# Kernel optimization log

Hardware: AMD Instinct MI355X
Metric: run time of the kernel (lower is better)

The kernel has to match this reference:

```python
import jax, jax.numpy as jnp
import numpy as np

B, CIN, COUT, K, H, W = 8, 512, 512, 3, 64, 64
SCALE = 1.0 / np.sqrt(CIN * K * K).astype(np.float32)  # conv.scale
LRELU_SCALE = 1.4142135623730951  # sqrt(2), FusedLeakyReLU scale


def setup_inputs() -> dict:
    key = jax.random.key(0)
    ks = jax.random.split(key, 6)
    return {
        "x": jax.random.normal(ks[0], (B, CIN, H, W), jnp.float32),
        "style": jax.random.normal(ks[1], (B, CIN), jnp.float32),
        "noise": jax.random.normal(ks[2], (1, 1, H, W), jnp.float32),
        "weight": jax.random.normal(ks[3], (COUT, CIN, K, K), jnp.float32),
        "bias": jnp.zeros((COUT,), jnp.float32),
        "noise_strength": jax.random.uniform(ks[4], (1,), jnp.float32),
    }


def reference(x, style, noise, weight, bias, noise_strength):
    # Modulate: scale * weight * style  -> [B, Cout, Cin, K, K]
    w = SCALE * weight[None] * style[:, None, :, None, None]
    # Demodulate per (batch, out_channel)
    demod = jax.lax.rsqrt(jnp.sum(w * w, axis=(2, 3, 4)) + 1e-8)
    w = w * demod[:, :, None, None, None]
    # Per-sample conv (grouped-conv trick in torch) via vmap over batch
    pad = K // 2
    def conv_one(xi, wi):  # xi: [Cin,H,W], wi: [Cout,Cin,K,K]
        return jax.lax.conv_general_dilated(
            xi[None], wi, window_strides=(1, 1),
            padding=[(pad, pad), (pad, pad)],
            dimension_numbers=("NCHW", "OIHW", "NCHW"))[0]
    out = jax.vmap(conv_one)(x, w)  # [B, Cout, H, W]
    # NoiseInjection: out + strength * noise (noise broadcast over B, C)
    out = out + noise_strength[0] * noise
    # FusedLeakyReLU: leaky_relu(out + bias, 0.2) * sqrt(2)
    y = out + bias[None, :, None, None]
    return jnp.where(y >= 0, y, 0.2 * y) * LRELU_SCALE
```

## Files before the change

kernel.cpp:

```cpp
#include <hip/hip_runtime.h>
#include <hip/hip_bf16.h>

typedef __attribute__((ext_vector_type(8))) short s16x8;
typedef __attribute__((ext_vector_type(16))) float f32x16;

#define MOD_SCALE 0.014731391274719739f

__device__ __forceinline__ void gload_lds16(const void* g, void* l) {
    __builtin_amdgcn_global_load_lds(
        (const __attribute__((address_space(1))) unsigned int*)g,
        (__attribute__((address_space(3))) unsigned int*)l, 16, 0, 0);
}

__device__ __forceinline__ void sync_drain() {
    __builtin_amdgcn_s_waitcnt(0);
    __syncthreads();
}

__global__ __launch_bounds__(256) void k_prep(const float* __restrict__ x,
                                              const float* __restrict__ style,
                                              const float* __restrict__ weight,
                                              __hip_bfloat16* __restrict__ xs,
                                              __hip_bfloat16* __restrict__ wb,
                                              float* __restrict__ dem) {
    __shared__ __align__(16) char sm[19456];
    const int t = threadIdx.x;
    const int bid = blockIdx.x;

    if (bid < 512) {
        const int b = bid >> 6, h = bid & 63;
        __hip_bfloat16 (*tile)[68] = (__hip_bfloat16(*)[68])sm;
        float* sf = (float*)(sm + 17408);
        sf[t] = style[b * 512 + t] * MOD_SCALE;
        sf[t + 256] = style[b * 512 + 256 + t] * MOD_SCALE;
        const float* xb = x + (size_t)b * 512 * 4096 + h * 64;
        const int cig = t & 3, w = t >> 2;
        char* ob = (char*)xs + (size_t)b * 4460544 +
                   (size_t)((h + 1) * 66 + 1) * 64;
        __syncthreads();
#pragma unroll
        for (int cq = 0; cq < 4; ++cq) {
#pragma unroll 4
            for (int it = 0; it < 8; ++it) {
                int idx = it * 256 + t;
                int cil = idx >> 4, w4 = idx & 15;
                int ci = cq * 128 + cil;
                float4 v = *(const float4*)(xb + (size_t)ci * 4096 + w4 * 4);
                float s = sf[ci];
                union { uint2 u2; __hip_bfloat16 q[4]; } pk;
                pk.q[0] = __float2bfloat16(v.x * s);
                pk.q[1] = __float2bfloat16(v.y * s);
                pk.q[2] = __float2bfloat16(v.z * s);
                pk.q[3] = __float2bfloat16(v.w * s);
                *(uint2*)&tile[cil][w4 * 4] = pk.u2;
            }
            __syncthreads();
#pragma unroll
            for (int cbl = 0; cbl < 4; ++cbl) {
                const int cb = cq * 4 + cbl;
                union { uint4 u; __hip_bfloat16 q[8]; } pk;
#pragma unroll
                for (int j = 0; j < 8; ++j)
                    pk.q[j] = tile[cbl * 32 + cig * 8 + j][w];
                *(uint4*)(ob + (size_t)cb * 278784 + w * 64 + cig * 16) = pk.u;
            }
            __syncthreads();
        }
    } else if (bid < 1032) {
        const int idx = (bid - 512) * 256 + t;
        const int b = idx / 16640;
        const int r2 = idx - b * 16640;
        const int cb = r2 / 1040;
        const int r3 = r2 - cb * 1040;
        const int pair = r3 >> 2;
        const int chunk = r3 & 3;
        int pr, pc;
        if (pair < 66)       { pr = 0;          pc = pair; }
        else if (pair < 132) { pr = 65;         pc = pair - 66; }
        else if (pair < 196) { pr = pair - 131; pc = 0; }
        else                 { pr = pair - 195; pc = 65; }
        char* d = (char*)xs +
                  ((size_t)(b * 16 + cb) * 4356 + pr * 66 + pc) * 64 +
                  chunk * 16;
        *(uint4*)d = make_uint4(0u, 0u, 0u, 0u);
    } else if (bid < 2056) {
        const int r = bid - 1032;
        float* lds = (float*)sm;
        const int p0 = r * 256;
        const float* src = weight + (size_t)p0 * 9;
#pragma unroll
        for (int k = 0; k < 9; ++k) lds[k * 256 + t] = src[k * 256 + t];
        __syncthreads();
#pragma unroll
        for (int tap = 0; tap < 9; ++tap)
            wb[(size_t)tap * 262144 + p0 + t] = __float2bfloat16(lds[t * 9 + tap]);
    } else {
        const int co = bid - 2056;
        float* s2 = (float*)sm;
        for (int i = t; i < 4096; i += 256) { float v = style[i]; s2[i] = v * v; }
        __syncthreads();
        const float4* wp = (const float4*)(weight + (size_t)co * 4608);
        float acc[8] = {0.f, 0.f, 0.f, 0.f, 0.f, 0.f, 0.f, 0.f};
        for (int j = t; j < 1152; j += 256) {
            float4 v = wp[j];
            float w2[4] = {v.x * v.x, v.y * v.y, v.z * v.z, v.w * v.w};
            int base = j * 4;
#pragma unroll
            for (int e = 0; e < 4; ++e) {
                int ci = (base + e) / 9;
                float ww = w2[e];
#pragma unroll
                for (int bb = 0; bb < 8; ++bb) acc[bb] += ww * s2[bb * 512 + ci];
            }
        }
#pragma unroll
        for (int bb = 0; bb < 8; ++bb)
            for (int off = 32; off > 0; off >>= 1)
                acc[bb] += __shfl_down(acc[bb], off);
        float* red = (float*)(sm + 16384);
        const int wv = t >> 6, lane = t & 63;
        if (lane == 0) {
#pragma unroll
            for (int bb = 0; bb < 8; ++bb) red[wv * 8 + bb] = acc[bb];
        }
        __syncthreads();
        if (t < 8) {
            float s = red[t] + red[8 + t] + red[16 + t] + red[24 + t];
            const float S2 = MOD_SCALE * MOD_SCALE;
            dem[t * 512 + co] = rsqrtf(S2 * s + 1e-8f);
        }
    }
}

__global__ __launch_bounds__(256, 2) void k_conv(
    const __hip_bfloat16* __restrict__ xs,
    const __hip_bfloat16* __restrict__ wb,
    const float* __restrict__ demod,
    const float* __restrict__ noise,
    const float* __restrict__ bias,
    const float* __restrict__ nstr,
    float* __restrict__ out) {
    __shared__ __align__(16) char Xl[25344];
    __shared__ __align__(16) char Wl[6][8192];

    const int t = threadIdx.x;
    const int bi = blockIdx.x;
    const int spat = bi & 127;
    const int b = spat >> 4;
    const int h0 = (spat & 15) << 2;
    const int co0 = (bi >> 7) << 7;
    const int lane = t & 63;
    const int wv = t >> 6;
    const int wm = wv & 1, wn = wv >> 1;
    const int el = lane & 31;
    const int hk = lane >> 5;

    f32x16 acc[2][4];
#pragma unroll
    for (int i = 0; i < 2; ++i)
#pragma unroll
        for (int j = 0; j < 4; ++j)
#pragma unroll
            for (int k = 0; k < 16; ++k) acc[i][j][k] = 0.f;

    const char* xsb = (const char*)xs + (size_t)b * 4460544;
    const char* xsrc[7];
#pragma unroll
    for (int i = 0; i < 6; ++i) {
        int g = i * 256 + t;
        int e = g >> 2, s = g & 3;
        int gc = (s - (e >> 2)) & 3;
        int row = e / 66, col = e - row * 66;
        xsrc[i] = xsb + (size_t)((h0 + row) * 66 + col) * 64 + gc * 16;
    }
    {
        int g = 1536 + t;
        int e = g >> 2, s = g & 3;
        int gc = (s - (e >> 2)) & 3;
        int row = e / 66, col = e - row * 66;
        xsrc[6] = xsb + (size_t)((h0 + row) * 66 + col) * 64 + gc * 16;
    }
    const char* wsrc[2];
#pragma unroll
    for (int i = 0; i < 2; ++i) {
        int g = i * 256 + t;
        int e = g >> 2, s = g & 3;
        int gc = (s - (e >> 2)) & 3;
        wsrc[i] = (const char*)wb + (size_t)(co0 + e) * 1024 + gc * 16;
    }
    const int wvoff = wv << 10;

#pragma unroll
    for (int i = 0; i < 6; ++i) gload_lds16(xsrc[i], Xl + i * 4096 + wvoff);
    if (t < 48) gload_lds16(xsrc[6], Xl + 24576);
#pragma unroll
    for (int tt = 0; tt < 3; ++tt)
#pragma unroll
        for (int i = 0; i < 2; ++i)
            gload_lds16(wsrc[i] + (size_t)tt * 524288,
                        Wl[tt] + i * 4096 + wvoff);
    sync_drain();

    int cboff = 0;
    for (int cb = 0; cb < 16; ++cb, cboff += 64) {
        const int ncboff = (cb < 15) ? cboff + 64 : cboff;
#pragma unroll
        for (int p = 0; p < 3; ++p) {
            const int bank = ((cb + p) & 1) * 3;
            const int nbank = 3 - bank;
#pragma unroll
            for (int tt = 0; tt < 3; ++tt) {
                const size_t soff = (p < 2)
                    ? (size_t)(3 * (p + 1) + tt) * 524288 + cboff
                    : (size_t)tt * 524288 + ncboff;
                char* dst = Wl[nbank + tt] + wvoff;
#pragma unroll
                for (int i = 0; i < 2; ++i)
                    gload_lds16(wsrc[i] + soff, dst + i * 4096);
            }
#pragma unroll
            for (int tt = 0; tt < 3; ++tt) {
                const char* Wb = Wl[bank + tt];
#pragma unroll
                for (int ks = 0; ks < 2; ++ks) {
                    const int c = 2 * ks + hk;
                    s16x8 af[2], bfr[4];
#pragma unroll
                    for (int mi = 0; mi < 2; ++mi) {
                        int e = wm * 64 + mi * 32 + el;
                        af[mi] = *(const s16x8*)(Wb + e * 64 +
                                                 (((c + (e >> 2)) & 3) << 4));
                    }
#pragma unroll
                    for (int ni = 0; ni < 4; ++ni) {
                        int e = (2 * wn + (ni >> 1) + p) * 66 + tt +
                                (ni & 1) * 32 + el;
                        bfr[ni] = *(const s16x8*)(Xl + e * 64 +
                                                  (((c + (e >> 2)) & 3) << 4));
                    }
#pragma unroll
                    for (int mi = 0; mi < 2; ++mi)
#pragma unroll
                        for (int ni = 0; ni < 4; ++ni)
                            acc[mi][ni] =
                                __builtin_amdgcn_mfma_f32_32x32x16_bf16(
                                    af[mi], bfr[ni], acc[mi][ni], 0, 0, 0);
                }
            }
            sync_drain();
        }
        if (cb < 15) {
            const size_t xo = (size_t)(cb + 1) * 278784;
#pragma unroll
            for (int i = 0; i < 6; ++i)
                gload_lds16(xsrc[i] + xo, Xl + i * 4096 + wvoff);
            if (t < 48) gload_lds16(xsrc[6] + xo, Xl + 24576);
            sync_drain();
        }
    }

    const float nsv = nstr[0];
    const float LR = 1.4142135623730951f;
#pragma unroll
    for (int mi = 0; mi < 2; ++mi) {
        float dm[16], bs[16];
#pragma unroll
        for (int rg = 0; rg < 16; ++rg) {
            int co = co0 + wm * 64 + mi * 32 + (rg & 3) + 8 * (rg >> 2) + 4 * hk;
            dm[rg] = demod[b * 512 + co];
            bs[rg] = bias[co];
        }
#pragma unroll
        for (int ni = 0; ni < 4; ++ni) {
            int h = h0 + 2 * wn + (ni >> 1);
            int w = (ni & 1) * 32 + el;
            float nz = nsv * noise[h * 64 + w];
#pragma unroll
            for (int rg = 0; rg < 16; ++rg) {
                int co = co0 + wm * 64 + mi * 32 + (rg & 3) + 8 * (rg >> 2) +
                         4 * hk;
                float v = acc[mi][ni][rg] * dm[rg] + nz + bs[rg];
                v = (v >= 0.f ? v : 0.2f * v) * LR;
                out[(((size_t)b * 512 + co) * 64 + h) * 64 + w] = v;
            }
        }
    }
}

extern "C" void kernel_launch(void* const* d_in, const int* in_sizes, int n_in,
                              void* d_out, int out_size, void* d_ws, size_t ws_size,
                              hipStream_t stream) {
    const float* x      = (const float*)d_in[0];
    const float* style  = (const float*)d_in[1];
    const float* noise  = (const float*)d_in[2];
    const float* weight = (const float*)d_in[3];
    const float* bias   = (const float*)d_in[4];
    const float* nstr   = (const float*)d_in[5];
    float* out = (float*)d_out;

    char* ws = (char*)d_ws;
    __hip_bfloat16* xs = (__hip_bfloat16*)ws;
    __hip_bfloat16* wb = (__hip_bfloat16*)(ws + 35684352);
    float* demod = (float*)(ws + 35684352 + 4718592);

    k_prep<<<2568, 256, 0, stream>>>(x, style, weight, xs, wb, demod);
    k_conv<<<512, 256, 0, stream>>>(xs, wb, demod, noise, bias, nstr, out);
}
```

Measured before the change: 250.3 us.

## Double-buffer input tile and pipeline weight taps with partial vmcnt barriers

The input-channel tile in LDS is now double-buffered, so the next block's activations load while the current block computes. The exposed full-drain X reload at the end of each channel block goes away. Weights move to a 3-slot ring with one tap prefetched two steps ahead. Full waitcnt(0) barriers are replaced with partial vmcnt waits so that outstanding loads overlap with MFMA work. The ring needs exact vmcnt accounting, which makes correctness fragile, and it uses more barriers, one per tap instead of one per row of three taps.

```diff
diff --git a/kernel.cpp b/kernel.cpp
--- a/kernel.cpp
+++ b/kernel.cpp
@@ -15,6 +15,19 @@
 __device__ __forceinline__ void sync_drain() {
     __builtin_amdgcn_s_waitcnt(0);
     __syncthreads();
+}
+
+__device__ __forceinline__ void bar_vm8() {
+    asm volatile("s_waitcnt vmcnt(8) lgkmcnt(0)" ::: "memory");
+    __builtin_amdgcn_sched_barrier(0);
+    __builtin_amdgcn_s_barrier();
+    __builtin_amdgcn_sched_barrier(0);
+}
+__device__ __forceinline__ void bar_vm2() {
+    asm volatile("s_waitcnt vmcnt(2) lgkmcnt(0)" ::: "memory");
+    __builtin_amdgcn_sched_barrier(0);
+    __builtin_amdgcn_s_barrier();
+    __builtin_amdgcn_sched_barrier(0);
 }
 
 __global__ __launch_bounds__(256) void k_prep(const float* __restrict__ x,
@@ -140,8 +153,8 @@
     const float* __restrict__ bias,
     const float* __restrict__ nstr,
     float* __restrict__ out) {
-    __shared__ __align__(16) char Xl[25344];
-    __shared__ __align__(16) char Wl[6][8192];
+    __shared__ __align__(16) char Xl[2][25344];
+    __shared__ __align__(16) char Wl[3][8192];
 
     const int t = threadIdx.x;
     const int bi = blockIdx.x;
@@ -191,71 +204,67 @@
     const int wvoff = wv << 10;
 
 #pragma unroll
-    for (int i = 0; i < 6; ++i) gload_lds16(xsrc[i], Xl + i * 4096 + wvoff);
-    if (t < 48) gload_lds16(xsrc[6], Xl + 24576);
-#pragma unroll
-    for (int tt = 0; tt < 3; ++tt)
+    for (int i = 0; i < 6; ++i) gload_lds16(xsrc[i], Xl[0] + i * 4096 + wvoff);
+    if (t < 48) gload_lds16(xsrc[6], Xl[0] + 24576);
+#pragma unroll
+    for (int tt = 0; tt < 2; ++tt)
 #pragma unroll
         for (int i = 0; i < 2; ++i)
             gload_lds16(wsrc[i] + (size_t)tt * 524288,
                         Wl[tt] + i * 4096 + wvoff);
     sync_drain();
 
-    int cboff = 0;
-    for (int cb = 0; cb < 16; ++cb, cboff += 64) {
+    for (int cb = 0; cb < 16; ++cb) {
+        const char* Xr = Xl[cb & 1];
+        char* Xw = Xl[(cb + 1) & 1];
+        const size_t xo = (size_t)(cb < 15 ? cb + 1 : cb) * 278784;
+#pragma unroll
+        for (int i = 0; i < 6; ++i)
+            gload_lds16(xsrc[i] + xo, Xw + i * 4096 + wvoff);
+        if (t < 48) gload_lds16(xsrc[6] + xo, Xw + 24576);
+
+        const int cboff = cb * 64;
         const int ncboff = (cb < 15) ? cboff + 64 : cboff;
 #pragma unroll
-        for (int p = 0; p < 3; ++p) {
-            const int bank = ((cb + p) & 1) * 3;
-            const int nbank = 3 - bank;
-#pragma unroll
-            for (int tt = 0; tt < 3; ++tt) {
-                const size_t soff = (p < 2)
-                    ? (size_t)(3 * (p + 1) + tt) * 524288 + cboff
-                    : (size_t)tt * 524288 + ncboff;
-                char* dst = Wl[nbank + tt] + wvoff;
+        for (int tap = 0; tap < 9; ++tap) {
+            {
+                const size_t soff =
+                    (tap < 7) ? (size_t)(tap + 2) * 524288 + cboff
+                              : (tap == 7 ? (size_t)ncboff
+                                          : (size_t)524288 + ncboff);
+                char* dst = Wl[(tap + 2) % 3] + wvoff;
 #pragma unroll
                 for (int i = 0; i < 2; ++i)
                     gload_lds16(wsrc[i] + soff, dst + i * 4096);
             }
-#pragma unroll
-            for (int tt = 0; tt < 3; ++tt) {
-                const char* Wb = Wl[bank + tt];
-#pragma unroll
-                for (int ks = 0; ks < 2; ++ks) {
-                    const int c = 2 * ks + hk;
-                    s16x8 af[2], bfr[4];
-#pragma unroll
-                    for (int mi = 0; mi < 2; ++mi) {
-                        int e = wm * 64 + mi * 32 + el;
-                        af[mi] = *(const s16x8*)(Wb + e * 64 +
-                                                 (((c + (e >> 2)) & 3) << 4));
-                    }
-#pragma unroll
-                    for (int ni = 0; ni < 4; ++ni) {
-                        int e = (2 * wn + (ni >> 1) + p) * 66 + tt +
-                                (ni & 1) * 32 + el;
-                        bfr[ni] = *(const s16x8*)(Xl + e * 64 +
-                                                  (((c + (e >> 2)) & 3) << 4));
-                    }
-#pragma unroll
-                    for (int mi = 0; mi < 2; ++mi)
-#pragma unroll
-                        for (int ni = 0; ni < 4; ++ni)
-                            acc[mi][ni] =
-                                __builtin_amdgcn_mfma_f32_32x32x16_bf16(
-                                    af[mi], bfr[ni], acc[mi][ni], 0, 0, 0);
+            const int dh = tap / 3, dw = tap % 3;
+            const char* Wb = Wl[tap % 3];
+#pragma unroll
+            for (int ks = 0; ks < 2; ++ks) {
+                const int c = 2 * ks + hk;
+                s16x8 af[2], bfr[4];
+#pragma unroll
+                for (int mi = 0; mi < 2; ++mi) {
+                    int e = wm * 64 + mi * 32 + el;
+                    af[mi] = *(const s16x8*)(Wb + e * 64 +
+                                             (((c + (e >> 2)) & 3) << 4));
                 }
-            }
-            sync_drain();
-        }
-        if (cb < 15) {
-            const size_t xo = (size_t)(cb + 1) * 278784;
-#pragma unroll
-            for (int i = 0; i < 6; ++i)
-                gload_lds16(xsrc[i] + xo, Xl + i * 4096 + wvoff);
-            if (t < 48) gload_lds16(xsrc[6] + xo, Xl + 24576);
-            sync_drain();
+#pragma unroll
+                for (int ni = 0; ni < 4; ++ni) {
+                    int e = (2 * wn + (ni >> 1) + dh) * 66 + dw +
+                            (ni & 1) * 32 + el;
+                    bfr[ni] = *(const s16x8*)(Xr + e * 64 +
+                                              (((c + (e >> 2)) & 3) << 4));
+                }
+#pragma unroll
+                for (int mi = 0; mi < 2; ++mi)
+#pragma unroll
+                    for (int ni = 0; ni < 4; ++ni)
+                        acc[mi][ni] = __builtin_amdgcn_mfma_f32_32x32x16_bf16(
+                            af[mi], bfr[ni], acc[mi][ni], 0, 0, 0);
+            }
+            if (tap == 0) bar_vm8();
+            else          bar_vm2();
         }
     }
 
```

Measured after the change: 287.9 us. 15.0% more time.
